# Optimization experiments

Measured on AMD Instinct MI355X. Metric: run time of the kernel, lower is better.

The kernel has to match this reference:

```python
import jax, jax.numpy as jnp
import numpy as np
import math

PI = math.pi
PHI = (1.0 + math.sqrt(5.0)) / 2.0
D_MODEL = 1024
N_HEADS = 16
D_HEAD = D_MODEL // N_HEADS
LAYER_DEPTH = 0.5
LAYER_INDEX = 0
CONV_RATE = 0.1


def setup_inputs() -> dict:
    key = jax.random.key(0)
    ks = jax.random.split(key, 5)
    B, T = 2, 2048
    x = jax.random.normal(ks[0], (B, T, D_MODEL), dtype=jnp.float32)
    s = 1.0 / math.sqrt(D_MODEL)
    Wq = jax.random.normal(ks[1], (D_MODEL, D_MODEL), dtype=jnp.float32) * s
    Wk = jax.random.normal(ks[2], (D_MODEL, D_MODEL), dtype=jnp.float32) * s
    Wv = jax.random.normal(ks[3], (D_MODEL, D_MODEL), dtype=jnp.float32) * s
    We = jax.random.normal(ks[4], (D_MODEL, D_MODEL), dtype=jnp.float32) * s
    # per-head chamber init, matching ApertureChamber / _head_depth
    frac = jnp.arange(N_HEADS, dtype=jnp.float32) / max(N_HEADS - 1, 1)
    lo = LAYER_DEPTH * 0.5
    hi = 0.5 + LAYER_DEPTH * 0.5
    depth = lo + frac * (hi - lo)
    beta = 0.5 + 0.2 * (1.0 - 2.0 * depth)           # [H] raw (pre-sigmoid) params
    input_valve = jnp.full((N_HEADS,), 0.5, dtype=jnp.float32)
    output_valve = jnp.full((N_HEADS,), 0.5, dtype=jnp.float32)
    chi = jnp.ones((N_HEADS,), dtype=jnp.float32)
    return {"x": x, "Wq": Wq, "Wk": Wk, "Wv": Wv, "We": We,
            "beta": beta, "input_valve": input_valve,
            "output_valve": output_valve, "chi": chi}


def reference(x, Wq, Wk, Wv, We, beta, input_valve, output_valve, chi):
    B, T, D = x.shape
    H, dh = N_HEADS, D // N_HEADS
    conv_factor = 1.0 / PHI ** (LAYER_INDEX * CONV_RATE)
    scale = math.sqrt(dh * conv_factor)
    # QKV projections (torch Linear: x @ W.T), split heads -> [B,H,T,dh]
    q = (x @ Wq.T).reshape(B, T, H, dh).transpose(0, 2, 1, 3)
    k = (x @ Wk.T).reshape(B, T, H, dh).transpose(0, 2, 1, 3)
    v = (x @ Wv.T).reshape(B, T, H, dh).transpose(0, 2, 1, 3)
    attn = jax.nn.softmax(jnp.einsum('bhqd,bhkd->bhqk', q, k) / scale, axis=-1)
    converged = jnp.einsum('bhqk,bhkd->bhqd', attn, v)  # [B,H,T,dh]
    # ApertureChamber per head, vectorized over H (broadcast [H] -> [1,H,1,1])
    b = jax.nn.sigmoid(beta)[None, :, None, None]
    iv = jax.nn.sigmoid(input_valve)[None, :, None, None]
    ov = jax.nn.sigmoid(output_valve)[None, :, None, None]
    g = jnp.tanh(chi)[None, :, None, None]
    ang = PI * b
    ca, sa = jnp.cos(ang), jnp.sin(ang)
    x_in = converged * iv
    half = dh // 2  # d_head even -> no leftover lane
    xr, xi = x_in[..., :half], x_in[..., half:]
    rot = jnp.concatenate([xr * ca - xi * sa, xr * sa + xi * ca], axis=-1)
    out = rot * ov * g  # output valve + tanh(chi) gate
    combined = out.transpose(0, 2, 1, 3).reshape(B, T, D)
    return combined @ We.T
```

## Files before the change

kernel.cpp:

```cpp
#include <hip/hip_runtime.h>
#include <hip/hip_bf16.h>
#include <math.h>

typedef __bf16 bf16;
typedef __bf16 bf16x4 __attribute__((ext_vector_type(4)));
typedef __bf16 bf16x8 __attribute__((ext_vector_type(8)));
typedef float f32x4 __attribute__((ext_vector_type(4)));
typedef float f32x16 __attribute__((ext_vector_type(16)));
typedef unsigned int u32x4 __attribute__((ext_vector_type(4)));

static __device__ __forceinline__ f32x4 mfma16(bf16x8 a, bf16x8 b, f32x4 c) {
  return __builtin_amdgcn_mfma_f32_16x16x32_bf16(a, b, c, 0, 0, 0);
}
static __device__ __forceinline__ f32x16 mfma32(bf16x8 a, bf16x8 b, f32x16 c) {
  return __builtin_amdgcn_mfma_f32_32x32x16_bf16(a, b, c, 0, 0, 0);
}
static __device__ __forceinline__ void gld_lds16(const void* g, void* l) {
  __builtin_amdgcn_global_load_lds(
      (const __attribute__((address_space(1))) void*)g,
      (__attribute__((address_space(3))) void*)l, 16, 0, 0);
}
static __device__ __forceinline__ unsigned cvt_pk_bf16(float lo, float hi) {
  unsigned r;
  asm("v_cvt_pk_bf16_f32 %0, %1, %2" : "=v"(r) : "v"(lo), "v"(hi));
  return r;
}

__global__ void cast_all(const float* __restrict__ x, const float* __restrict__ Wq,
                         const float* __restrict__ Wk, const float* __restrict__ Wv,
                         const float* __restrict__ We,
                         bf16* __restrict__ xb, bf16* __restrict__ qb,
                         bf16* __restrict__ kb, bf16* __restrict__ vb,
                         bf16* __restrict__ eb) {
  int i = blockIdx.x * 256 + threadIdx.x;
  const float* s; bf16* d; int off;
  if (i < 1048576) { s = x; d = xb; off = i; }
  else {
    int j = i - 1048576; int w = j >> 18; off = j & 262143;
    s = (w == 0) ? Wq : (w == 1) ? Wk : (w == 2) ? Wv : We;
    d = (w == 0) ? qb : (w == 1) ? kb : (w == 2) ? vb : eb;
  }
  float4 v = reinterpret_cast<const float4*>(s)[off];
  bf16x4 o; o[0] = (bf16)v.x; o[1] = (bf16)v.y; o[2] = (bf16)v.z; o[3] = (bf16)v.w;
  reinterpret_cast<bf16x4*>(d)[off] = o;
}

template<int MODE>
__global__ void gemm_bt(const bf16* __restrict__ A,
                        const bf16* __restrict__ B0, const bf16* __restrict__ B1,
                        const bf16* __restrict__ B2,
                        void* __restrict__ C0v, void* __restrict__ C1v, void* __restrict__ C2v,
                        int M, int N, int K) {
  __shared__ bf16 As[128 * 32];
  __shared__ bf16 Bs[128 * 32];
  const int tid = threadIdx.x;
  const int wave = tid >> 6;
  const int lane = tid & 63;
  const int bid = blockIdx.x | (blockIdx.y << 3) | (blockIdx.z << 8);
  const int cpx = gridDim.z << 5;
  const int swz = (bid & 7) * cpx + (bid >> 3);
  const int n0 = (swz & 7) * 128;
  const int m0 = ((swz >> 3) & 31) * 128;
  const int zz = swz >> 8;
  const bf16* B = (zz == 0) ? B0 : (zz == 1) ? B1 : B2;
  void* Cv = (zz == 0) ? C0v : (zz == 1) ? C1v : C2v;
  const int wr = (wave >> 1) * 64;
  const int wc = (wave & 1) * 64;
  const int frow = lane & 15;
  const int fk = (lane >> 4) * 8;
  const int arow = wave * 16 + (lane >> 2);
  const int acol = (lane & 3) * 8;
  f32x4 acc[4][4] = {};
  char* AsB = (char*)As;
  char* BsB = (char*)Bs;
  for (int k0 = 0; k0 < K; k0 += 32) {
    __syncthreads();
    gld_lds16(&A[(size_t)(m0 + arow) * K + k0 + acol],      AsB + wave * 1024);
    gld_lds16(&A[(size_t)(m0 + 64 + arow) * K + k0 + acol], AsB + 4096 + wave * 1024);
    gld_lds16(&B[(size_t)(n0 + arow) * K + k0 + acol],      BsB + wave * 1024);
    gld_lds16(&B[(size_t)(n0 + 64 + arow) * K + k0 + acol], BsB + 4096 + wave * 1024);
    asm volatile("s_waitcnt vmcnt(0)" ::: "memory");
    __syncthreads();
    bf16x8 af[4], bfr[4];
#pragma unroll
    for (int mi = 0; mi < 4; ++mi)
      af[mi] = *reinterpret_cast<const bf16x8*>(&As[(wr + mi * 16 + frow) * 32 + fk]);
#pragma unroll
    for (int ni = 0; ni < 4; ++ni)
      bfr[ni] = *reinterpret_cast<const bf16x8*>(&Bs[(wc + ni * 16 + frow) * 32 + fk]);
    __builtin_amdgcn_s_setprio(1);
#pragma unroll
    for (int mi = 0; mi < 4; ++mi)
#pragma unroll
      for (int ni = 0; ni < 4; ++ni)
        acc[mi][ni] = mfma16(af[mi], bfr[ni], acc[mi][ni]);
    __builtin_amdgcn_s_setprio(0);
  }
#pragma unroll
  for (int mi = 0; mi < 4; ++mi) {
#pragma unroll
    for (int ni = 0; ni < 4; ++ni) {
#pragma unroll
      for (int r = 0; r < 4; ++r) {
        int row = m0 + wr + mi * 16 + (lane >> 4) * 4 + r;
        int col = n0 + wc + ni * 16 + frow;
        if (MODE == 0) {
          int b = row >> 11, t = row & 2047, h = col >> 6, d = col & 63;
          ((bf16*)Cv)[(((size_t)b * 16 + h) * 2048 + t) * 64 + d] = (bf16)acc[mi][ni][r];
        } else {
          ((float*)Cv)[(size_t)row * N + col] = acc[mi][ni][r];
        }
      }
    }
  }
}

__global__ void transpose_v(const bf16* __restrict__ v, bf16* __restrict__ vt) {
  __shared__ bf16 tile[64][65];
  int bh = blockIdx.y;
  int t0 = blockIdx.x * 64;
  for (int idx = threadIdx.x; idx < 64 * 64; idx += 256) {
    int r = idx >> 6, c = idx & 63;
    tile[r][c] = v[((size_t)bh * 2048 + t0 + r) * 64 + c];
  }
  __syncthreads();
  for (int idx = threadIdx.x; idx < 64 * 64; idx += 256) {
    int d = idx >> 6, r = idx & 63;
    vt[((size_t)bh * 64 + d) * 2048 + t0 + r] = tile[r][d];
  }
}

__global__ void attn_kernel(const bf16* __restrict__ q, const bf16* __restrict__ k,
                            const bf16* __restrict__ vt,
                            const float* __restrict__ beta, const float* __restrict__ ivp,
                            const float* __restrict__ ovp, const float* __restrict__ chip,
                            bf16* __restrict__ comb) {
  __shared__ bf16 Ks[2][64 * 64];
  __shared__ bf16 Vs[2][64 * 64];
  __shared__ float red[4][32];
  const int tid = threadIdx.x;
  const int wave = tid >> 6, lane = tid & 63;
  const int hi = lane >> 5, ln = lane & 31;
  const int bid = blockIdx.x | (blockIdx.y << 4);
  const int swz = (bid & 7) * 64 + (bid >> 3);
  const int qblk = swz & 15, bh = swz >> 4;
  const int h = bh & 15, b = bh >> 4;
  const int q0w = qblk * 128 + wave * 32;
  const float C = 0.18033688011112042f;

  const bf16* qrow = q + ((size_t)bh * 2048 + q0w + ln) * 64 + hi * 8;
  bf16x8 qf[4];
#pragma unroll
  for (int ds = 0; ds < 4; ++ds)
    qf[ds] = *reinterpret_cast<const bf16x8*>(qrow + ds * 16);

  const bf16* kbase = k + (size_t)bh * 2048 * 64;
  const bf16* vbase = vt + (size_t)bh * 64 * 2048;
  const int srow = lane >> 3;
  const int scol = ((lane & 7) ^ (srow & 7)) * 8;

  f32x16 acc0 = {}, acc1 = {};
  float m_run = -1e30f, l_run = 0.f;

  auto stage = [&](int buf, int k0) {
#pragma unroll
    for (int j = 0; j < 2; ++j) {
      int u = wave * 2 + j;
      int r = u * 8 + srow;
      gld_lds16(&kbase[(size_t)(k0 + r) * 64 + scol], (char*)&Ks[buf][0] + u * 1024);
      gld_lds16(&vbase[(size_t)r * 2048 + k0 + scol], (char*)&Vs[buf][0] + u * 1024);
    }
  };

  stage(0, 0);
  int cur = 0;
  for (int k0 = 0; k0 < 2048; k0 += 64) {
    asm volatile("s_waitcnt vmcnt(0)" ::: "memory");
    __syncthreads();
    if (k0 + 64 < 2048) stage(cur ^ 1, k0 + 64);

    f32x16 s[2];
    s[0] = (f32x16){}; s[1] = (f32x16){};
    const char* kb = (const char*)&Ks[cur][0];
    __builtin_amdgcn_s_setprio(1);
#pragma unroll
    for (int kh = 0; kh < 2; ++kh) {
      const int r = kh * 32 + ln;
      const int rx = (r & 7) << 4;
#pragma unroll
      for (int ds = 0; ds < 4; ++ds) {
        bf16x8 kf = *reinterpret_cast<const bf16x8*>(kb + r * 128 + ((ds * 32 + hi * 16) ^ rx));
        s[kh] = mfma32(kf, qf[ds], s[kh]);
      }
    }
    __builtin_amdgcn_s_setprio(0);

    float tm = -1e30f;
#pragma unroll
    for (int kh = 0; kh < 2; ++kh)
#pragma unroll
      for (int r = 0; r < 16; ++r) tm = fmaxf(tm, s[kh][r]);
    tm = fmaxf(tm, __shfl_xor(tm, 32));
    if (!__all(tm - m_run <= 64.f)) {
      float mnew = fmaxf(m_run, tm);
      float e = exp2f((m_run - mnew) * C);
      if (hi == 0) red[wave][ln] = e;
      asm volatile("s_waitcnt lgkmcnt(0)" ::: "memory");
#pragma unroll
      for (int r = 0; r < 16; ++r) {
        float er = red[wave][(r & 3) + 8 * (r >> 2) + 4 * hi];
        acc0[r] *= er; acc1[r] *= er;
      }
      l_run *= e;
      m_run = mnew;
    }
    float mC = m_run * C;
    float psum = 0.f;
#pragma unroll
    for (int kh = 0; kh < 2; ++kh)
#pragma unroll
      for (int r = 0; r < 16; ++r) {
        float p = exp2f(fmaf(s[kh][r], C, -mC));
        s[kh][r] = p;
        psum += p;
      }
    psum += __shfl_xor(psum, 32);
    l_run += psum;

    const char* vb = (const char*)&Vs[cur][0];
#pragma unroll
    for (int ks = 0; ks < 4; ++ks) {
      const int kh = ks >> 1;
      const int b0 = 8 * (ks & 1);
      unsigned a0 = cvt_pk_bf16(s[kh][b0 + 0], s[kh][b0 + 1]);
      unsigned a1 = cvt_pk_bf16(s[kh][b0 + 4], s[kh][b0 + 5]);
      unsigned c0 = cvt_pk_bf16(s[kh][b0 + 2], s[kh][b0 + 3]);
      unsigned c1 = cvt_pk_bf16(s[kh][b0 + 6], s[kh][b0 + 7]);
      asm("v_permlane32_swap_b32 %0, %1" : "+v"(a0), "+v"(a1));
      asm("v_permlane32_swap_b32 %0, %1" : "+v"(c0), "+v"(c1));
      union { u32x4 u; bf16x8 v; } pf;
      pf.u[0] = a0; pf.u[1] = c0; pf.u[2] = a1; pf.u[3] = c1;
      __builtin_amdgcn_s_setprio(1);
#pragma unroll
      for (int dh = 0; dh < 2; ++dh) {
        const int r = dh * 32 + ln;
        bf16x8 vf = *reinterpret_cast<const bf16x8*>(
            vb + r * 128 + ((ks * 32 + hi * 16) ^ ((r & 7) << 4)));
        if (dh == 0) acc0 = mfma32(pf.v, vf, acc0);
        else         acc1 = mfma32(pf.v, vf, acc1);
      }
      __builtin_amdgcn_s_setprio(0);
    }
    cur ^= 1;
  }

  if (hi == 0) red[wave][ln] = 1.f / l_run;
  asm volatile("s_waitcnt lgkmcnt(0)" ::: "memory");
  float bb = 1.f / (1.f + expf(-beta[h]));
  float ang = 3.14159265358979323846f * bb;
  float ca = cosf(ang), sa = sinf(ang);
  float iv = 1.f / (1.f + expf(-ivp[h]));
  float ov = 1.f / (1.f + expf(-ovp[h]));
  float g = tanhf(chip[h]);
  float K1 = iv * ov * g * ca;
  float K2 = iv * ov * g * sa;
#pragma unroll
  for (int r = 0; r < 16; ++r) {
    int qr = (r & 3) + 8 * (r >> 2) + 4 * hi;
    float inv = red[wave][qr];
    float o_r = acc0[r] * inv, o_i = acc1[r] * inv;
    size_t base = ((size_t)b * 2048 + q0w + qr) * 1024 + (size_t)h * 64;
    comb[base + ln]      = (bf16)(K1 * o_r - K2 * o_i);
    comb[base + 32 + ln] = (bf16)(K2 * o_r + K1 * o_i);
  }
}

extern "C" void kernel_launch(void* const* d_in, const int* in_sizes, int n_in,
                              void* d_out, int out_size, void* d_ws, size_t ws_size,
                              hipStream_t stream) {
  const float* x    = (const float*)d_in[0];
  const float* Wq   = (const float*)d_in[1];
  const float* Wk   = (const float*)d_in[2];
  const float* Wv   = (const float*)d_in[3];
  const float* We   = (const float*)d_in[4];
  const float* beta = (const float*)d_in[5];
  const float* ivp  = (const float*)d_in[6];
  const float* ovp  = (const float*)d_in[7];
  const float* chip = (const float*)d_in[8];

  char* ws = (char*)d_ws;
  bf16* x_bf  = (bf16*)(ws + (size_t)0);
  bf16* Wq_bf = (bf16*)(ws + ((size_t)8  << 20));
  bf16* Wk_bf = (bf16*)(ws + ((size_t)10 << 20));
  bf16* Wv_bf = (bf16*)(ws + ((size_t)12 << 20));
  bf16* We_bf = (bf16*)(ws + ((size_t)14 << 20));
  bf16* q_bf  = (bf16*)(ws + ((size_t)16 << 20));
  bf16* k_bf  = (bf16*)(ws + ((size_t)24 << 20));
  bf16* v_bf  = (bf16*)(ws + ((size_t)32 << 20));
  bf16* v_t   = (bf16*)(ws + ((size_t)40 << 20));
  bf16* comb  = (bf16*)(ws + ((size_t)48 << 20));

  cast_all<<<8192, 256, 0, stream>>>(x, Wq, Wk, Wv, We, x_bf, Wq_bf, Wk_bf, Wv_bf, We_bf);

  gemm_bt<0><<<dim3(8, 32, 3), 256, 0, stream>>>(x_bf, Wq_bf, Wk_bf, Wv_bf,
                                                 q_bf, k_bf, v_bf, 4096, 1024, 1024);
  transpose_v<<<dim3(32, 32), 256, 0, stream>>>(v_bf, v_t);
  attn_kernel<<<dim3(16, 32), 256, 0, stream>>>(q_bf, k_bf, v_t, beta, ivp, ovp, chip, comb);
  gemm_bt<1><<<dim3(8, 32, 1), 256, 0, stream>>>(comb, We_bf, We_bf, We_bf,
                                                 d_out, d_out, d_out, 4096, 1024, 1024);
}
```

Before: 218.4 us.

## Double K-tile depth in GEMM and attention, swizzle LDS, use shuffles for softmax rescale

The GEMM now stages 64-wide K slices with an XOR-swizzled LDS layout, so there are half as many barrier and wait rounds per output tile. The attention kernel processes 128 keys per iteration, doubling the K/V LDS buffers and adding a 16-way swizzle for V. It replaces the LDS-based row broadcast of rescale and normalisation factors with lane shuffles, and reduces the max and sum with trees. The cost is more LDS and register pressure, which may lower occupancy.

New measurement: 260.4 us. +19.2%, slower.

```diff
diff --git a/kernel.cpp b/kernel.cpp
--- a/kernel.cpp
+++ b/kernel.cpp
@@ -24,6 +24,22 @@
   unsigned r;
   asm("v_cvt_pk_bf16_f32 %0, %1, %2" : "=v"(r) : "v"(lo), "v"(hi));
   return r;
+}
+static __device__ __forceinline__ float rmax16(f32x16 v) {
+  float a0 = fmaxf(v[0], v[8]),  a1 = fmaxf(v[1], v[9]);
+  float a2 = fmaxf(v[2], v[10]), a3 = fmaxf(v[3], v[11]);
+  float a4 = fmaxf(v[4], v[12]), a5 = fmaxf(v[5], v[13]);
+  float a6 = fmaxf(v[6], v[14]), a7 = fmaxf(v[7], v[15]);
+  a0 = fmaxf(a0, a4); a1 = fmaxf(a1, a5); a2 = fmaxf(a2, a6); a3 = fmaxf(a3, a7);
+  return fmaxf(fmaxf(a0, a1), fmaxf(a2, a3));
+}
+static __device__ __forceinline__ float rsum16(f32x16 v) {
+  float a0 = v[0] + v[8],  a1 = v[1] + v[9];
+  float a2 = v[2] + v[10], a3 = v[3] + v[11];
+  float a4 = v[4] + v[12], a5 = v[5] + v[13];
+  float a6 = v[6] + v[14], a7 = v[7] + v[15];
+  a0 += a4; a1 += a5; a2 += a6; a3 += a7;
+  return (a0 + a1) + (a2 + a3);
 }
 
 __global__ void cast_all(const float* __restrict__ x, const float* __restrict__ Wq,
@@ -51,8 +67,8 @@
                         const bf16* __restrict__ B2,
                         void* __restrict__ C0v, void* __restrict__ C1v, void* __restrict__ C2v,
                         int M, int N, int K) {
-  __shared__ bf16 As[128 * 32];
-  __shared__ bf16 Bs[128 * 32];
+  __shared__ bf16 As[128 * 64];
+  __shared__ bf16 Bs[128 * 64];
   const int tid = threadIdx.x;
   const int wave = tid >> 6;
   const int lane = tid & 63;
@@ -67,34 +83,43 @@
   const int wr = (wave >> 1) * 64;
   const int wc = (wave & 1) * 64;
   const int frow = lane & 15;
-  const int fk = (lane >> 4) * 8;
-  const int arow = wave * 16 + (lane >> 2);
-  const int acol = (lane & 3) * 8;
+  const int fx = frow & 7;
+  const int khi = lane >> 4;
+  const int srow8 = lane >> 3;
+  const int scol = ((lane & 7) ^ srow8) * 8;
   f32x4 acc[4][4] = {};
   char* AsB = (char*)As;
   char* BsB = (char*)Bs;
-  for (int k0 = 0; k0 < K; k0 += 32) {
+  for (int k0 = 0; k0 < K; k0 += 64) {
     __syncthreads();
-    gld_lds16(&A[(size_t)(m0 + arow) * K + k0 + acol],      AsB + wave * 1024);
-    gld_lds16(&A[(size_t)(m0 + 64 + arow) * K + k0 + acol], AsB + 4096 + wave * 1024);
-    gld_lds16(&B[(size_t)(n0 + arow) * K + k0 + acol],      BsB + wave * 1024);
-    gld_lds16(&B[(size_t)(n0 + 64 + arow) * K + k0 + acol], BsB + 4096 + wave * 1024);
+#pragma unroll
+    for (int j = 0; j < 4; ++j) {
+      int u = j * 4 + wave;
+      int row = u * 8 + srow8;
+      gld_lds16(&A[(size_t)(m0 + row) * K + k0 + scol], AsB + u * 1024);
+      gld_lds16(&B[(size_t)(n0 + row) * K + k0 + scol], BsB + u * 1024);
+    }
     asm volatile("s_waitcnt vmcnt(0)" ::: "memory");
     __syncthreads();
-    bf16x8 af[4], bfr[4];
-#pragma unroll
-    for (int mi = 0; mi < 4; ++mi)
-      af[mi] = *reinterpret_cast<const bf16x8*>(&As[(wr + mi * 16 + frow) * 32 + fk]);
-#pragma unroll
-    for (int ni = 0; ni < 4; ++ni)
-      bfr[ni] = *reinterpret_cast<const bf16x8*>(&Bs[(wc + ni * 16 + frow) * 32 + fk]);
-    __builtin_amdgcn_s_setprio(1);
-#pragma unroll
-    for (int mi = 0; mi < 4; ++mi)
+#pragma unroll
+    for (int kk = 0; kk < 2; ++kk) {
+      bf16x8 af[4], bfr[4];
+#pragma unroll
+      for (int mi = 0; mi < 4; ++mi)
+        af[mi] = *reinterpret_cast<const bf16x8*>(
+            AsB + (wr + mi * 16 + frow) * 128 + (((kk << 2) + khi) ^ fx) * 16);
 #pragma unroll
       for (int ni = 0; ni < 4; ++ni)
-        acc[mi][ni] = mfma16(af[mi], bfr[ni], acc[mi][ni]);
-    __builtin_amdgcn_s_setprio(0);
+        bfr[ni] = *reinterpret_cast<const bf16x8*>(
+            BsB + (wc + ni * 16 + frow) * 128 + (((kk << 2) + khi) ^ fx) * 16);
+      __builtin_amdgcn_s_setprio(1);
+#pragma unroll
+      for (int mi = 0; mi < 4; ++mi)
+#pragma unroll
+        for (int ni = 0; ni < 4; ++ni)
+          acc[mi][ni] = mfma16(af[mi], bfr[ni], acc[mi][ni]);
+      __builtin_amdgcn_s_setprio(0);
+    }
   }
 #pragma unroll
   for (int mi = 0; mi < 4; ++mi) {
@@ -102,7 +127,7 @@
     for (int ni = 0; ni < 4; ++ni) {
 #pragma unroll
       for (int r = 0; r < 4; ++r) {
-        int row = m0 + wr + mi * 16 + (lane >> 4) * 4 + r;
+        int row = m0 + wr + mi * 16 + khi * 4 + r;
         int col = n0 + wc + ni * 16 + frow;
         if (MODE == 0) {
           int b = row >> 11, t = row & 2047, h = col >> 6, d = col & 63;
@@ -135,9 +160,8 @@
                             const float* __restrict__ beta, const float* __restrict__ ivp,
                             const float* __restrict__ ovp, const float* __restrict__ chip,
                             bf16* __restrict__ comb) {
-  __shared__ bf16 Ks[2][64 * 64];
-  __shared__ bf16 Vs[2][64 * 64];
-  __shared__ float red[4][32];
+  __shared__ bf16 Ks[2][128 * 64];
+  __shared__ bf16 Vs[2][64 * 128];
   const int tid = threadIdx.x;
   const int wave = tid >> 6, lane = tid & 63;
   const int hi = lane >> 5, ln = lane & 31;
@@ -156,86 +180,88 @@
 
   const bf16* kbase = k + (size_t)bh * 2048 * 64;
   const bf16* vbase = vt + (size_t)bh * 64 * 2048;
-  const int srow = lane >> 3;
-  const int scol = ((lane & 7) ^ (srow & 7)) * 8;
+  const int krow_off = lane >> 3;
+  const int kscol = ((lane & 7) ^ krow_off) * 8;
+  const int vd_off = lane >> 4;
+  const int vs = lane & 15;
 
   f32x16 acc0 = {}, acc1 = {};
   float m_run = -1e30f, l_run = 0.f;
 
   auto stage = [&](int buf, int k0) {
 #pragma unroll
-    for (int j = 0; j < 2; ++j) {
-      int u = wave * 2 + j;
-      int r = u * 8 + srow;
-      gld_lds16(&kbase[(size_t)(k0 + r) * 64 + scol], (char*)&Ks[buf][0] + u * 1024);
-      gld_lds16(&vbase[(size_t)r * 2048 + k0 + scol], (char*)&Vs[buf][0] + u * 1024);
+    for (int j = 0; j < 4; ++j) {
+      int u = j * 4 + wave;
+      int kr = u * 8 + krow_off;
+      gld_lds16(&kbase[(size_t)(k0 + kr) * 64 + kscol], (char*)&Ks[buf][0] + u * 1024);
+      int d = u * 4 + vd_off;
+      int vcol = (vs ^ (d & 15)) * 8;
+      gld_lds16(&vbase[(size_t)d * 2048 + k0 + vcol], (char*)&Vs[buf][0] + u * 1024);
     }
   };
 
   stage(0, 0);
   int cur = 0;
-  for (int k0 = 0; k0 < 2048; k0 += 64) {
+  for (int k0 = 0; k0 < 2048; k0 += 128) {
     asm volatile("s_waitcnt vmcnt(0)" ::: "memory");
     __syncthreads();
-    if (k0 + 64 < 2048) stage(cur ^ 1, k0 + 64);
-
-    f32x16 s[2];
-    s[0] = (f32x16){}; s[1] = (f32x16){};
+    if (k0 + 128 < 2048) stage(cur ^ 1, k0 + 128);
+
+    f32x16 s4[4];
     const char* kb = (const char*)&Ks[cur][0];
     __builtin_amdgcn_s_setprio(1);
 #pragma unroll
-    for (int kh = 0; kh < 2; ++kh) {
+    for (int kh = 0; kh < 4; ++kh) {
+      s4[kh] = (f32x16){};
       const int r = kh * 32 + ln;
       const int rx = (r & 7) << 4;
 #pragma unroll
       for (int ds = 0; ds < 4; ++ds) {
         bf16x8 kf = *reinterpret_cast<const bf16x8*>(kb + r * 128 + ((ds * 32 + hi * 16) ^ rx));
-        s[kh] = mfma32(kf, qf[ds], s[kh]);
+        s4[kh] = mfma32(kf, qf[ds], s4[kh]);
       }
     }
     __builtin_amdgcn_s_setprio(0);
 
-    float tm = -1e30f;
-#pragma unroll
-    for (int kh = 0; kh < 2; ++kh)
-#pragma unroll
-      for (int r = 0; r < 16; ++r) tm = fmaxf(tm, s[kh][r]);
+    f32x16 mx = __builtin_elementwise_max(
+        __builtin_elementwise_max(s4[0], s4[1]),
+        __builtin_elementwise_max(s4[2], s4[3]));
+    float tm = rmax16(mx);
     tm = fmaxf(tm, __shfl_xor(tm, 32));
     if (!__all(tm - m_run <= 64.f)) {
       float mnew = fmaxf(m_run, tm);
       float e = exp2f((m_run - mnew) * C);
-      if (hi == 0) red[wave][ln] = e;
-      asm volatile("s_waitcnt lgkmcnt(0)" ::: "memory");
 #pragma unroll
       for (int r = 0; r < 16; ++r) {
-        float er = red[wave][(r & 3) + 8 * (r >> 2) + 4 * hi];
+        int qr = (r & 3) + 8 * (r >> 2) + 4 * hi;
+        float er = __shfl(e, qr, 32);
         acc0[r] *= er; acc1[r] *= er;
       }
       l_run *= e;
       m_run = mnew;
     }
     float mC = m_run * C;
-    float psum = 0.f;
-#pragma unroll
-    for (int kh = 0; kh < 2; ++kh)
-#pragma unroll
-      for (int r = 0; r < 16; ++r) {
-        float p = exp2f(fmaf(s[kh][r], C, -mC));
-        s[kh][r] = p;
-        psum += p;
-      }
+    f32x16 ps = {};
+#pragma unroll
+    for (int kh = 0; kh < 4; ++kh) {
+      f32x16 z = s4[kh] * C - mC;
+#pragma unroll
+      for (int e = 0; e < 16; ++e) s4[kh][e] = exp2f(z[e]);
+      ps += s4[kh];
+    }
+    float psum = rsum16(ps);
     psum += __shfl_xor(psum, 32);
     l_run += psum;
 
     const char* vb = (const char*)&Vs[cur][0];
 #pragma unroll
-    for (int ks = 0; ks < 4; ++ks) {
+    for (int ks = 0; ks < 8; ++ks) {
       const int kh = ks >> 1;
       const int b0 = 8 * (ks & 1);
-      unsigned a0 = cvt_pk_bf16(s[kh][b0 + 0], s[kh][b0 + 1]);
-      unsigned a1 = cvt_pk_bf16(s[kh][b0 + 4], s[kh][b0 + 5]);
-      unsigned c0 = cvt_pk_bf16(s[kh][b0 + 2], s[kh][b0 + 3]);
-      unsigned c1 = cvt_pk_bf16(s[kh][b0 + 6], s[kh][b0 + 7]);
+      unsigned a0 = cvt_pk_bf16(s4[kh][b0 + 0], s4[kh][b0 + 1]);
+      unsigned a1 = cvt_pk_bf16(s4[kh][b0 + 4], s4[kh][b0 + 5]);
+      unsigned c0 = cvt_pk_bf16(s4[kh][b0 + 2], s4[kh][b0 + 3]);
+      unsigned c1 = cvt_pk_bf16(s4[kh][b0 + 6], s4[kh][b0 + 7]);
       asm("v_permlane32_swap_b32 %0, %1" : "+v"(a0), "+v"(a1));
       asm("v_permlane32_swap_b32 %0, %1" : "+v"(c0), "+v"(c1));
       union { u32x4 u; bf16x8 v; } pf;
@@ -245,7 +271,7 @@
       for (int dh = 0; dh < 2; ++dh) {
         const int r = dh * 32 + ln;
         bf16x8 vf = *reinterpret_cast<const bf16x8*>(
-            vb + r * 128 + ((ks * 32 + hi * 16) ^ ((r & 7) << 4)));
+            vb + r * 256 + (((2 * ks + hi) ^ (r & 15))) * 16);
         if (dh == 0) acc0 = mfma32(pf.v, vf, acc0);
         else         acc1 = mfma32(pf.v, vf, acc1);
       }
@@ -254,8 +280,7 @@
     cur ^= 1;
   }
 
-  if (hi == 0) red[wave][ln] = 1.f / l_run;
-  asm volatile("s_waitcnt lgkmcnt(0)" ::: "memory");
+  float inv = 1.f / l_run;
   float bb = 1.f / (1.f + expf(-beta[h]));
   float ang = 3.14159265358979323846f * bb;
   float ca = cosf(ang), sa = sinf(ang);
@@ -267,8 +292,8 @@
 #pragma unroll
   for (int r = 0; r < 16; ++r) {
     int qr = (r & 3) + 8 * (r >> 2) + 4 * hi;
-    float inv = red[wave][qr];
-    float o_r = acc0[r] * inv, o_i = acc1[r] * inv;
+    float iq = __shfl(inv, qr, 32);
+    float o_r = acc0[r] * iq, o_i = acc1[r] * iq;
     size_t base = ((size_t)b * 2048 + q0w + qr) * 1024 + (size_t)h * 64;
     comb[base + ln]      = (bf16)(K1 * o_r - K2 * o_i);
     comb[base + 32 + ln] = (bf16)(K2 * o_r + K1 * o_i);
```
